# Optimization experiments

Measured on AMD Instinct MI355X. Metric: run time of the kernel, lower is better.

The kernel has to match this reference:

```python
import jax, jax.numpy as jnp
import numpy as np

SUBSTEP = 10
FRAMES = 24
T = FRAMES * SUBSTEP
DT = 1.0 / 60.0 / SUBSTEP
SLOPE_DEG = 20.0
COS_S = float(np.cos(np.deg2rad(SLOPE_DEG)))
SIN_S = float(np.sin(np.deg2rad(SLOPE_DEG)))
INIT_HEIGHT = 0.1
N_VERTS = 2_000_000
GRAVITY = jnp.array([0.0, -9.8, 0.0], dtype=jnp.float32)
CONTACT_N = jnp.array([-SIN_S, COS_S, 0.0], dtype=jnp.float32)
EPS = 1e-6


def quat_mul(a, b):
    w1, x1, y1, z1 = a[0], a[1], a[2], a[3]
    w2, x2, y2, z2 = b[0], b[1], b[2], b[3]
    return jnp.stack([
        w1 * w2 - x1 * x2 - y1 * y2 - z1 * z2,
        w1 * x2 + x1 * w2 + y1 * z2 - z1 * y2,
        w1 * y2 + y1 * w2 + z1 * x2 - x1 * z2,
        w1 * z2 + z1 * w2 + x1 * y2 - y1 * x2,
    ])


def quat_to_matrix(q):
    q = q / jnp.linalg.norm(q)
    w, x, y, z = q[0], q[1], q[2], q[3]
    return jnp.stack([
        jnp.stack([1 - 2 * y * y - 2 * z * z, 2 * x * y - 2 * w * z, 2 * x * z + 2 * w * y]),
        jnp.stack([2 * x * y + 2 * w * z, 1 - 2 * x * x - 2 * z * z, 2 * y * z - 2 * w * x]),
        jnp.stack([2 * x * z - 2 * w * y, 2 * y * z + 2 * w * x, 1 - 2 * x * x - 2 * y * y]),
    ])


def cross_matrix(a):
    z = jnp.zeros((), dtype=a.dtype)
    return jnp.stack([
        jnp.stack([z, -a[2], a[1]]),
        jnp.stack([a[2], z, -a[0]]),
        jnp.stack([-a[1], a[0], z]),
    ])


def setup_inputs() -> dict:
    key = jax.random.key(0)
    k1, k2, k3 = jax.random.split(key, 3)
    return {
        "x": jax.random.normal(k1, (N_VERTS, 3), dtype=jnp.float32) * 0.2,
        "mass_center": jnp.zeros((3,), dtype=jnp.float32),
        "init_trans": jax.random.normal(k2, (3,), dtype=jnp.float32) * 0.3 + jnp.array([0.3, 0.5, 0.0]),
        "init_quat": jnp.ones((4,), dtype=jnp.float32),
        "init_v": jax.random.normal(k3, (3,), dtype=jnp.float32) * 0.1,
        "kn": jnp.array([0.5], dtype=jnp.float32),
        "mu": jnp.array([0.4], dtype=jnp.float32),
        "linear_damping": jnp.array([0.999], dtype=jnp.float32),
        "angular_damping": jnp.array([0.998], dtype=jnp.float32),
    }


def _simulate(x, mass_center, init_trans, init_quat, init_v, kn, mu, linear_damping, angular_damping):
    n = x.shape[0]
    mass = jnp.asarray(float(n), dtype=x.dtype)  # unit mass per vertex
    inv_mass = 1.0 / mass
    r = x - mass_center
    # inertia_reference = sum_i m*( (r.r) I - outer(r,r) )
    inertia = jnp.sum(jnp.einsum('ni,ni->n', r, r)) * jnp.eye(3, dtype=x.dtype) - jnp.einsum('ni,nj->ij', r, r)
    kn0, mu0 = kn[0], mu[0]
    ld, ad = linear_damping[0], angular_damping[0]
    eye3 = jnp.eye(3, dtype=x.dtype)

    def step(carry, _):
        trans, quat, v, omega = carry
        Rm = quat_to_matrix(quat)
        Rx = x @ Rm.T                                   # [N,3]
        xi = trans + Rx + mass_center                   # world positions
        vi_all = v + jnp.cross(omega[None, :], Rx)      # per-vertex velocities
        d = xi @ CONTACT_N
        rel_v = vi_all @ CONTACT_N
        mask = (d < -COS_S * INIT_HEIGHT) & (rel_v < 0.0)
        num = jnp.sum(mask)
        numf = jnp.maximum(num, 1).astype(x.dtype)
        sum_pos = jnp.sum(x * mask[:, None].astype(x.dtype), axis=0)
        ri = sum_pos / numf
        Ri = Rm @ ri
        vi = v + jnp.cross(omega, Ri)
        v_n = jnp.dot(vi, CONTACT_N) * CONTACT_N
        v_t = vi - v_n
        vn_new = -kn0 * v_n
        alpha = jnp.maximum(1.0 - mu0 * (1.0 + kn0) * (jnp.linalg.norm(v_n) / (jnp.linalg.norm(v_t) + EPS)), 0.0)
        vi_new = vn_new + alpha * v_t
        I = Rm @ inertia @ Rm.T
        I_inv = jnp.linalg.inv(I)
        Rri = cross_matrix(Ri)
        kmat = inv_mass * eye3 - Rri @ I_inv @ Rri
        J = jnp.linalg.solve(kmat, vi_new - vi)
        hit = num > 0
        dv = jnp.where(hit, J * inv_mass, 0.0)
        domega = jnp.where(hit, I_inv @ Rri @ J, 0.0)
        v_new = (v + GRAVITY * DT) * ld + dv
        omega_new = omega * ad + domega
        trans_new = trans + DT * v_new
        wq = jnp.concatenate([jnp.zeros((1,), dtype=x.dtype), omega_new]) * (0.5 * DT)
        quat_new = quat + quat_mul(wq, quat)
        quat_new = quat_new / jnp.linalg.norm(quat_new)
        new_carry = (trans_new, quat_new, v_new, omega_new)
        return new_carry, jnp.concatenate([trans_new, quat_new])

    carry0 = (init_trans, init_quat / jnp.linalg.norm(init_quat), init_v, jnp.zeros(3, dtype=x.dtype))
    _, traj = jax.lax.scan(step, carry0, None, length=T)
    return traj  # [T, 7] = translation(3) + quaternion(4) per substep


def reference(x, mass_center, init_trans, init_quat, init_v, kn, mu, linear_damping, angular_damping):
    return _simulate(x, mass_center, init_trans, init_quat, init_v, kn, mu, linear_damping, angular_damping)
```

## Files before the change

kernel.cpp:

```cpp
#include <hip/hip_runtime.h>

#define GRID    256
#define BLOCK   512
#define NWAVES  (BLOCK / 64)
#define CHUNK   7813

typedef unsigned long long u64;

__device__ __forceinline__ u64 rec_load(const u64* p) {
  return __hip_atomic_load(p, __ATOMIC_RELAXED, __HIP_MEMORY_SCOPE_AGENT);
}
__device__ __forceinline__ void rec_store(u64* p, u64 v) {
  __hip_atomic_store(p, v, __ATOMIC_RELAXED, __HIP_MEMORY_SCOPE_AGENT);
}
__device__ __forceinline__ u64 rec_pack(float f, unsigned tag) {
  return (u64)__float_as_uint(f) | ((u64)tag << 32);
}

template <int NV>
__device__ __forceinline__ void block_reduce(float* v, float* sm) {
  #pragma unroll
  for (int off = 32; off > 0; off >>= 1) {
    #pragma unroll
    for (int k = 0; k < NV; ++k) v[k] += __shfl_down(v[k], off, 64);
  }
  const int lane = threadIdx.x & 63;
  const int wid  = threadIdx.x >> 6;
  if (lane == 0) {
    #pragma unroll
    for (int k = 0; k < NV; ++k) sm[wid * NV + k] = v[k];
  }
  __syncthreads();
  if (threadIdx.x == 0) {
    #pragma unroll
    for (int w = 1; w < NWAVES; ++w) {
      #pragma unroll
      for (int k = 0; k < NV; ++k) v[k] += sm[w * NV + k];
    }
  }
  __syncthreads();
}

__device__ __forceinline__ void mat3_mul(const float* A, const float* B, float* C) {
  #pragma unroll
  for (int i = 0; i < 3; ++i)
    #pragma unroll
    for (int j = 0; j < 3; ++j)
      C[i*3+j] = A[i*3+0]*B[0*3+j] + A[i*3+1]*B[1*3+j] + A[i*3+2]*B[2*3+j];
}
__device__ __forceinline__ void mat3_mul_bt(const float* A, const float* B, float* C) {
  #pragma unroll
  for (int i = 0; i < 3; ++i)
    #pragma unroll
    for (int j = 0; j < 3; ++j)
      C[i*3+j] = A[i*3+0]*B[j*3+0] + A[i*3+1]*B[j*3+1] + A[i*3+2]*B[j*3+2];
}
__device__ __forceinline__ void mat3_inv(const float* m, float* inv) {
  float A =  (m[4]*m[8] - m[5]*m[7]);
  float B = -(m[3]*m[8] - m[5]*m[6]);
  float C =  (m[3]*m[7] - m[4]*m[6]);
  float det = m[0]*A + m[1]*B + m[2]*C;
  float id = 1.0f / det;
  inv[0] = A * id;
  inv[1] = -(m[1]*m[8] - m[2]*m[7]) * id;
  inv[2] =  (m[1]*m[5] - m[2]*m[4]) * id;
  inv[3] = B * id;
  inv[4] =  (m[0]*m[8] - m[2]*m[6]) * id;
  inv[5] = -(m[0]*m[5] - m[2]*m[3]) * id;
  inv[6] = C * id;
  inv[7] = -(m[0]*m[7] - m[1]*m[6]) * id;
  inv[8] =  (m[0]*m[4] - m[1]*m[3]) * id;
}

__global__ __launch_bounds__(BLOCK)
void sim_kernel(const float* __restrict__ xg,
                const float* __restrict__ mc_p,
                const float* __restrict__ itr_p,
                const float* __restrict__ iq_p,
                const float* __restrict__ iv_p,
                const float* __restrict__ kn_p,
                const float* __restrict__ mu_p,
                const float* __restrict__ ldp_p,
                const float* __restrict__ adp_p,
                float* __restrict__ out,
                u64* __restrict__ ws,
                int N, int T)
{
  const int tid = threadIdx.x;
  const int bid = blockIdx.x;

  extern __shared__ float dyn[];
  float* sXx = dyn;
  float* sXy = dyn + CHUNK;
  float* sXz = dyn + 2 * CHUNK;
  __shared__ float s_red[NWAVES * 8];
  __shared__ float s_plane[8];

  const float nx  = (float)(-0.3420201433256687);
  const float ny  = (float)( 0.9396926207859084);
  const float DTF = (float)(1.0 / 60.0 / 10.0);
  const float HDT = (float)(0.5 * (1.0 / 60.0 / 10.0));
  const float DTH = (float)(-0.9396926207859084 * 0.1);
  const float GYDT = -9.8f * (float)(1.0 / 60.0 / 10.0);

  const float mc0 = mc_p[0], mc1 = mc_p[1], mc2 = mc_p[2];

  u64* part0 = ws;
  u64* part1 = ws + 4 * GRID;
  u64* st    = ws + 8 * GRID;
  u64* bufI  = ws + 8 * GRID + 128;

  const int vstart = bid * CHUNK;
  int cl = N - vstart; if (cl > CHUNK) cl = CHUNK; if (cl < 0) cl = 0;

  for (int i = tid; i < cl; i += BLOCK) {
    const float* p = xg + (size_t)(vstart + i) * 3;
    sXx[i] = p[0]; sXy[i] = p[1]; sXz[i] = p[2];
  }
  __syncthreads();

  {
    float v6[6] = {0,0,0,0,0,0};
    for (int i = tid; i < cl; i += BLOCK) {
      float r0 = sXx[i] - mc0, r1 = sXy[i] - mc1, r2 = sXz[i] - mc2;
      v6[0] += r0*r0; v6[1] += r1*r1; v6[2] += r2*r2;
      v6[3] += r0*r1; v6[4] += r0*r2; v6[5] += r1*r2;
    }
    block_reduce<6>(v6, s_red);
    if (tid == 0) {
      #pragma unroll
      for (int k = 0; k < 6; ++k) rec_store(bufI + k * GRID + bid, rec_pack(v6[k], 0xC0FFEEu));
    }
  }

  float In[9];
  if (bid == 0) {
    float v6[6] = {0,0,0,0,0,0};
    if (tid < GRID) {
      u64 r[6];
      int f = 0;
      for (;;) {
        #pragma unroll
        for (int k = 0; k < 6; ++k) r[k] = rec_load(bufI + k * GRID + tid);
        bool ok = true;
        #pragma unroll
        for (int k = 0; k < 6; ++k) ok &= ((unsigned)(r[k] >> 32) == 0xC0FFEEu);
        if (ok) break;
        if ((++f & 15) == 0) __builtin_amdgcn_s_sleep(1);
      }
      #pragma unroll
      for (int k = 0; k < 6; ++k) v6[k] = __uint_as_float((unsigned)r[k]);
    }
    block_reduce<6>(v6, s_red);
    float trc = v6[0] + v6[1] + v6[2];
    In[0] = trc - v6[0]; In[4] = trc - v6[1]; In[8] = trc - v6[2];
    In[1] = -v6[3]; In[3] = -v6[3];
    In[2] = -v6[4]; In[6] = -v6[4];
    In[5] = -v6[5]; In[7] = -v6[5];
  }

  float tr0 = itr_p[0], tr1 = itr_p[1], tr2 = itr_p[2];
  float q0 = iq_p[0], q1 = iq_p[1], q2 = iq_p[2], q3 = iq_p[3];
  {
    float n0 = sqrtf(q0*q0 + q1*q1 + q2*q2 + q3*q3);
    q0 /= n0; q1 /= n0; q2 /= n0; q3 /= n0;
  }
  float v0 = iv_p[0], v1 = iv_p[1], v2 = iv_p[2];
  float om0 = 0.f, om1 = 0.f, om2 = 0.f;
  const float knv = kn_p[0], muv = mu_p[0], ldv = ldp_p[0], adv = adp_p[0];
  const float inv_mass = 1.0f / (float)N;

  float Rm[9];
  float Ii[9];

  if (tid == 0) {
    float qn = sqrtf(q0*q0 + q1*q1 + q2*q2 + q3*q3);
    float w = q0/qn, xq = q1/qn, yq = q2/qn, zq = q3/qn;
    Rm[0] = 1.f - 2.f*yq*yq - 2.f*zq*zq; Rm[1] = 2.f*xq*yq - 2.f*w*zq; Rm[2] = 2.f*xq*zq + 2.f*w*yq;
    Rm[3] = 2.f*xq*yq + 2.f*w*zq; Rm[4] = 1.f - 2.f*xq*xq - 2.f*zq*zq; Rm[5] = 2.f*yq*zq - 2.f*w*xq;
    Rm[6] = 2.f*xq*zq - 2.f*w*yq; Rm[7] = 2.f*yq*zq + 2.f*w*xq; Rm[8] = 1.f - 2.f*xq*xq - 2.f*yq*yq;
    float a0 = Rm[0]*nx + Rm[3]*ny;
    float a1 = Rm[1]*nx + Rm[4]*ny;
    float a2 = Rm[2]*nx + Rm[5]*ny;
    float w0 = ny*om2, w1 = -nx*om2, w2 = nx*om1 - ny*om0;
    float b0 = Rm[0]*w0 + Rm[3]*w1 + Rm[6]*w2;
    float b1 = Rm[1]*w0 + Rm[4]*w1 + Rm[7]*w2;
    float b2 = Rm[2]*w0 + Rm[5]*w1 + Rm[8]*w2;
    float ca = DTH - ((tr0 + mc0)*nx + (tr1 + mc1)*ny);
    float cb = -(v0*nx + v1*ny);
    s_plane[0] = a0; s_plane[1] = a1; s_plane[2] = a2;
    s_plane[3] = b0; s_plane[4] = b1; s_plane[5] = b2;
    s_plane[6] = ca; s_plane[7] = cb;
    if (bid == 0) {
      float Tm[9]; mat3_mul(Rm, In, Tm);
      float Iw[9]; mat3_mul_bt(Tm, Rm, Iw);
      mat3_inv(Iw, Ii);
    }
  }
  __syncthreads();

  for (int t = 0; t < T; ++t) {
    const float a0 = s_plane[0], a1 = s_plane[1], a2 = s_plane[2];
    const float b0 = s_plane[3], b1 = s_plane[4], b2 = s_plane[5];
    const float ca = s_plane[6], cb = s_plane[7];

    float acc[4] = {0.f, 0.f, 0.f, 0.f};
    for (int i = tid; i < cl; i += BLOCK) {
      float x0 = sXx[i], x1 = sXy[i], x2 = sXz[i];
      float da = x0*a0 + x1*a1 + x2*a2;
      float db = x0*b0 + x1*b1 + x2*b2;
      if (da < ca && db < cb) { acc[0] += 1.f; acc[1] += x0; acc[2] += x1; acc[3] += x2; }
    }
    block_reduce<4>(acc, s_red);

    const unsigned want = (unsigned)(t + 1);
    u64* pb = (t & 1) ? part1 : part0;
    if (tid == 0) {
      #pragma unroll
      for (int k = 0; k < 4; ++k) rec_store(pb + k * GRID + bid, rec_pack(acc[k], want));
    }

    if (bid == 0) {
      float tot[4] = {0.f, 0.f, 0.f, 0.f};
      if (tid < GRID) {
        u64 r0, r1, r2, r3;
        int f = 0;
        for (;;) {
          r0 = rec_load(pb + 0 * GRID + tid);
          r1 = rec_load(pb + 1 * GRID + tid);
          r2 = rec_load(pb + 2 * GRID + tid);
          r3 = rec_load(pb + 3 * GRID + tid);
          if ((unsigned)(r0 >> 32) == want && (unsigned)(r1 >> 32) == want &&
              (unsigned)(r2 >> 32) == want && (unsigned)(r3 >> 32) == want) break;
          if ((++f & 15) == 0) __builtin_amdgcn_s_sleep(1);
        }
        tot[0] = __uint_as_float((unsigned)r0);
        tot[1] = __uint_as_float((unsigned)r1);
        tot[2] = __uint_as_float((unsigned)r2);
        tot[3] = __uint_as_float((unsigned)r3);
      }
      block_reduce<4>(tot, s_red);

      if (tid == 0) {
        float num = tot[0];
        float numf = fmaxf(num, 1.0f);
        float ri0 = tot[1] / numf, ri1 = tot[2] / numf, ri2 = tot[3] / numf;
        float Ri0 = Rm[0]*ri0 + Rm[1]*ri1 + Rm[2]*ri2;
        float Ri1 = Rm[3]*ri0 + Rm[4]*ri1 + Rm[5]*ri2;
        float Ri2 = Rm[6]*ri0 + Rm[7]*ri1 + Rm[8]*ri2;
        float dv0 = 0.f, dv1 = 0.f, dv2 = 0.f, dm0 = 0.f, dm1 = 0.f, dm2 = 0.f;
        if (num > 0.0f) {
          float vi0 = v0 + om1*Ri2 - om2*Ri1;
          float vi1 = v1 + om2*Ri0 - om0*Ri2;
          float vi2 = v2 + om0*Ri1 - om1*Ri0;
          float vdn = vi0*nx + vi1*ny;
          float vn0 = vdn*nx, vn1 = vdn*ny;
          float vt0 = vi0 - vn0, vt1 = vi1 - vn1, vt2 = vi2;
          float nvn = sqrtf(vn0*vn0 + vn1*vn1);
          float nvt = sqrtf(vt0*vt0 + vt1*vt1 + vt2*vt2);
          float alpha = fmaxf(1.0f - muv*(1.0f + knv)*(nvn/(nvt + 1e-6f)), 0.0f);
          float dvi0 = (-knv*vn0 + alpha*vt0) - vi0;
          float dvi1 = (-knv*vn1 + alpha*vt1) - vi1;
          float dvi2 = (alpha*vt2) - vi2;
          float Cx[9] = {0.f, -Ri2, Ri1,  Ri2, 0.f, -Ri0,  -Ri1, Ri0, 0.f};
          float T2[9]; mat3_mul(Cx, Ii, T2);
          float T3[9]; mat3_mul(T2, Cx, T3);
          float K[9];
          #pragma unroll
          for (int k = 0; k < 9; ++k) K[k] = -T3[k];
          K[0] += inv_mass; K[4] += inv_mass; K[8] += inv_mass;
          float Ki[9]; mat3_inv(K, Ki);
          float J0 = Ki[0]*dvi0 + Ki[1]*dvi1 + Ki[2]*dvi2;
          float J1 = Ki[3]*dvi0 + Ki[4]*dvi1 + Ki[5]*dvi2;
          float J2 = Ki[6]*dvi0 + Ki[7]*dvi1 + Ki[8]*dvi2;
          dv0 = J0*inv_mass; dv1 = J1*inv_mass; dv2 = J2*inv_mass;
          float c0 = -Ri2*J1 + Ri1*J2;
          float c1 =  Ri2*J0 - Ri0*J2;
          float c2 = -Ri1*J0 + Ri0*J1;
          dm0 = Ii[0]*c0 + Ii[1]*c1 + Ii[2]*c2;
          dm1 = Ii[3]*c0 + Ii[4]*c1 + Ii[5]*c2;
          dm2 = Ii[6]*c0 + Ii[7]*c1 + Ii[8]*c2;
        }
        v0 = v0*ldv + dv0;
        v1 = (v1 + GYDT)*ldv + dv1;
        v2 = v2*ldv + dv2;
        om0 = om0*adv + dm0; om1 = om1*adv + dm1; om2 = om2*adv + dm2;
        tr0 = tr0 + DTF*v0; tr1 = tr1 + DTF*v1; tr2 = tr2 + DTF*v2;
        float wx = om0*HDT, wy = om1*HDT, wz = om2*HDT;
        float dq0 = -wx*q1 - wy*q2 - wz*q3;
        float dq1 =  wx*q0 + wy*q3 - wz*q2;
        float dq2 =  wy*q0 + wz*q1 - wx*q3;
        float dq3 =  wz*q0 + wx*q2 - wy*q1;
        q0 += dq0; q1 += dq1; q2 += dq2; q3 += dq3;
        float qn2 = sqrtf(q0*q0 + q1*q1 + q2*q2 + q3*q3);
        q0 /= qn2; q1 /= qn2; q2 /= qn2; q3 /= qn2;
        float* o = out + (size_t)t * 7;
        o[0] = tr0; o[1] = tr1; o[2] = tr2;
        o[3] = q0;  o[4] = q1;  o[5] = q2;  o[6] = q3;
        float qn = sqrtf(q0*q0 + q1*q1 + q2*q2 + q3*q3);
        float w = q0/qn, xq = q1/qn, yq = q2/qn, zq = q3/qn;
        Rm[0] = 1.f - 2.f*yq*yq - 2.f*zq*zq; Rm[1] = 2.f*xq*yq - 2.f*w*zq; Rm[2] = 2.f*xq*zq + 2.f*w*yq;
        Rm[3] = 2.f*xq*yq + 2.f*w*zq; Rm[4] = 1.f - 2.f*xq*xq - 2.f*zq*zq; Rm[5] = 2.f*yq*zq - 2.f*w*xq;
        Rm[6] = 2.f*xq*zq - 2.f*w*yq; Rm[7] = 2.f*yq*zq + 2.f*w*xq; Rm[8] = 1.f - 2.f*xq*xq - 2.f*yq*yq;
        float na0 = Rm[0]*nx + Rm[3]*ny;
        float na1 = Rm[1]*nx + Rm[4]*ny;
        float na2 = Rm[2]*nx + Rm[5]*ny;
        float w0 = ny*om2, w1 = -nx*om2, w2 = nx*om1 - ny*om0;
        float nb0 = Rm[0]*w0 + Rm[3]*w1 + Rm[6]*w2;
        float nb1 = Rm[1]*w0 + Rm[4]*w1 + Rm[7]*w2;
        float nb2 = Rm[2]*w0 + Rm[5]*w1 + Rm[8]*w2;
        float nca = DTH - ((tr0 + mc0)*nx + (tr1 + mc1)*ny);
        float ncb = -(v0*nx + v1*ny);
        s_plane[0] = na0; s_plane[1] = na1; s_plane[2] = na2;
        s_plane[3] = nb0; s_plane[4] = nb1; s_plane[5] = nb2;
        s_plane[6] = nca; s_plane[7] = ncb;
      }
      __syncthreads();
      if (tid < 64) {
        u64* sl = st + (size_t)((t + 1) & 1) * 64;
        rec_store(sl + tid, rec_pack(s_plane[tid & 7], want));
      }
      if (tid == 0) {
        float Tm[9]; mat3_mul(Rm, In, Tm);
        float Iw[9]; mat3_mul_bt(Tm, Rm, Iw);
        mat3_inv(Iw, Ii);
      }
    } else {
      if (tid < 8) {
        const u64* sl = st + (size_t)((t + 1) & 1) * 64 + (size_t)(bid & 7) * 8;
        u64 r; int f = 0;
        for (;;) {
          r = rec_load(sl + tid);
          if ((unsigned)(r >> 32) == want) break;
          if ((++f & 31) == 0) __builtin_amdgcn_s_sleep(1);
        }
        s_plane[tid] = __uint_as_float((unsigned)r);
      }
      __syncthreads();
    }
  }
}

extern "C" void kernel_launch(void* const* d_in, const int* in_sizes, int n_in,
                              void* d_out, int out_size, void* d_ws, size_t ws_size,
                              hipStream_t stream) {
  const float* x   = (const float*)d_in[0];
  const float* mc  = (const float*)d_in[1];
  const float* itr = (const float*)d_in[2];
  const float* iq  = (const float*)d_in[3];
  const float* iv  = (const float*)d_in[4];
  const float* kn  = (const float*)d_in[5];
  const float* mu  = (const float*)d_in[6];
  const float* ldp = (const float*)d_in[7];
  const float* adp = (const float*)d_in[8];
  float* out = (float*)d_out;
  u64* ws  = (u64*)d_ws;
  int N = in_sizes[0] / 3;
  int T = out_size / 7;

  const int dyn_lds = 3 * CHUNK * 4;
  hipFuncSetAttribute((const void*)sim_kernel,
                      hipFuncAttributeMaxDynamicSharedMemorySize, dyn_lds);

  void* args[] = {(void*)&x, (void*)&mc, (void*)&itr, (void*)&iq, (void*)&iv,
                  (void*)&kn, (void*)&mu, (void*)&ldp, (void*)&adp,
                  (void*)&out, (void*)&ws, (void*)&N, (void*)&T};
  hipLaunchCooperativeKernel((void*)sim_kernel, dim3(GRID), dim3(BLOCK),
                             args, dyn_lds, stream);
}
```

Measured before the change: 1.469 ms.

## Dedicate block 0 to a single-wave coordinator, distribute vertices over remaining blocks

Block 0 no longer processes vertices. Its first wave polls all partial records, reduces them with wave shuffles, integrates the rigid body and publishes the next plane, with no __syncthreads or LDS round trips on the serial critical path. The other 255 blocks take slightly larger chunks to cover all vertices. This shortens the per-step serial latency between the global reduction and the broadcast, at the cost of one idle block and a little more work per compute block.

```diff
diff --git a/kernel.cpp b/kernel.cpp
--- a/kernel.cpp
+++ b/kernel.cpp
@@ -3,7 +3,7 @@
 #define GRID    256
 #define BLOCK   512
 #define NWAVES  (BLOCK / 64)
-#define CHUNK   7813
+#define CHUNK   7844
 
 typedef unsigned long long u64;
 
@@ -86,8 +86,10 @@
                 u64* __restrict__ ws,
                 int N, int T)
 {
-  const int tid = threadIdx.x;
-  const int bid = blockIdx.x;
+  const int tid  = threadIdx.x;
+  const int bid  = blockIdx.x;
+  const int lane = tid & 63;
+  const int wid  = tid >> 6;
 
   extern __shared__ float dyn[];
   float* sXx = dyn;
@@ -110,8 +112,9 @@
   u64* st    = ws + 8 * GRID;
   u64* bufI  = ws + 8 * GRID + 128;
 
-  const int vstart = bid * CHUNK;
-  int cl = N - vstart; if (cl > CHUNK) cl = CHUNK; if (cl < 0) cl = 0;
+  const int vstart = (bid - 1) * CHUNK;
+  int cl = 0;
+  if (bid > 0) { cl = N - vstart; if (cl > CHUNK) cl = CHUNK; if (cl < 0) cl = 0; }
 
   for (int i = tid; i < cl; i += BLOCK) {
     const float* p = xg + (size_t)(vstart + i) * 3;
@@ -199,133 +202,167 @@
   }
   __syncthreads();
 
-  for (int t = 0; t < T; ++t) {
-    const float a0 = s_plane[0], a1 = s_plane[1], a2 = s_plane[2];
-    const float b0 = s_plane[3], b1 = s_plane[4], b2 = s_plane[5];
-    const float ca = s_plane[6], cb = s_plane[7];
-
-    float acc[4] = {0.f, 0.f, 0.f, 0.f};
-    for (int i = tid; i < cl; i += BLOCK) {
-      float x0 = sXx[i], x1 = sXy[i], x2 = sXz[i];
-      float da = x0*a0 + x1*a1 + x2*a2;
-      float db = x0*b0 + x1*b1 + x2*b2;
-      if (da < ca && db < cb) { acc[0] += 1.f; acc[1] += x0; acc[2] += x1; acc[3] += x2; }
-    }
-    block_reduce<4>(acc, s_red);
-
-    const unsigned want = (unsigned)(t + 1);
-    u64* pb = (t & 1) ? part1 : part0;
-    if (tid == 0) {
-      #pragma unroll
-      for (int k = 0; k < 4; ++k) rec_store(pb + k * GRID + bid, rec_pack(acc[k], want));
-    }
-
-    if (bid == 0) {
-      float tot[4] = {0.f, 0.f, 0.f, 0.f};
-      if (tid < GRID) {
-        u64 r0, r1, r2, r3;
-        int f = 0;
-        for (;;) {
-          r0 = rec_load(pb + 0 * GRID + tid);
-          r1 = rec_load(pb + 1 * GRID + tid);
-          r2 = rec_load(pb + 2 * GRID + tid);
-          r3 = rec_load(pb + 3 * GRID + tid);
-          if ((unsigned)(r0 >> 32) == want && (unsigned)(r1 >> 32) == want &&
-              (unsigned)(r2 >> 32) == want && (unsigned)(r3 >> 32) == want) break;
-          if ((++f & 15) == 0) __builtin_amdgcn_s_sleep(1);
-        }
-        tot[0] = __uint_as_float((unsigned)r0);
-        tot[1] = __uint_as_float((unsigned)r1);
-        tot[2] = __uint_as_float((unsigned)r2);
-        tot[3] = __uint_as_float((unsigned)r3);
+  if (bid == 0) {
+    if (wid == 0) {
+      const int base = lane * 4;
+      for (int t = 0; t < T; ++t) {
+        const unsigned want = (unsigned)(t + 1);
+        u64* pb = (t & 1) ? part1 : part0;
+
+        u64 r0_[4], r1_[4], r2_[4], r3_[4];
+        {
+          int f = 0;
+          for (;;) {
+            #pragma unroll
+            for (int j = 0; j < 4; ++j) {
+              r0_[j] = rec_load(pb + 0 * GRID + base + j);
+              r1_[j] = rec_load(pb + 1 * GRID + base + j);
+              r2_[j] = rec_load(pb + 2 * GRID + base + j);
+              r3_[j] = rec_load(pb + 3 * GRID + base + j);
+            }
+            bool ok = true;
+            #pragma unroll
+            for (int j = 0; j < 4; ++j) {
+              bool skip = (base + j == 0);
+              ok &= skip || (((unsigned)(r0_[j] >> 32) == want) &&
+                             ((unsigned)(r1_[j] >> 32) == want) &&
+                             ((unsigned)(r2_[j] >> 32) == want) &&
+                             ((unsigned)(r3_[j] >> 32) == want));
+            }
+            if (__ballot(ok) == ~0ull) break;
+            if ((++f & 15) == 0) __builtin_amdgcn_s_sleep(1);
+          }
+        }
+        float s0 = 0.f, s1 = 0.f, s2 = 0.f, s3 = 0.f;
+        #pragma unroll
+        for (int j = 0; j < 4; ++j) {
+          if (base + j != 0) {
+            s0 += __uint_as_float((unsigned)r0_[j]);
+            s1 += __uint_as_float((unsigned)r1_[j]);
+            s2 += __uint_as_float((unsigned)r2_[j]);
+            s3 += __uint_as_float((unsigned)r3_[j]);
+          }
+        }
+        #pragma unroll
+        for (int off = 32; off > 0; off >>= 1) {
+          s0 += __shfl_down(s0, off, 64);
+          s1 += __shfl_down(s1, off, 64);
+          s2 += __shfl_down(s2, off, 64);
+          s3 += __shfl_down(s3, off, 64);
+        }
+
+        float pl0, pl1, pl2, pl3, pl4, pl5, pl6, pl7;
+        if (lane == 0) {
+          float num = s0;
+          float numf = fmaxf(num, 1.0f);
+          float ri0 = s1 / numf, ri1 = s2 / numf, ri2 = s3 / numf;
+          float Ri0 = Rm[0]*ri0 + Rm[1]*ri1 + Rm[2]*ri2;
+          float Ri1 = Rm[3]*ri0 + Rm[4]*ri1 + Rm[5]*ri2;
+          float Ri2 = Rm[6]*ri0 + Rm[7]*ri1 + Rm[8]*ri2;
+          float dv0 = 0.f, dv1 = 0.f, dv2 = 0.f, dm0 = 0.f, dm1 = 0.f, dm2 = 0.f;
+          if (num > 0.0f) {
+            float vi0 = v0 + om1*Ri2 - om2*Ri1;
+            float vi1 = v1 + om2*Ri0 - om0*Ri2;
+            float vi2 = v2 + om0*Ri1 - om1*Ri0;
+            float vdn = vi0*nx + vi1*ny;
+            float vn0 = vdn*nx, vn1 = vdn*ny;
+            float vt0 = vi0 - vn0, vt1 = vi1 - vn1, vt2 = vi2;
+            float nvn = sqrtf(vn0*vn0 + vn1*vn1);
+            float nvt = sqrtf(vt0*vt0 + vt1*vt1 + vt2*vt2);
+            float alpha = fmaxf(1.0f - muv*(1.0f + knv)*(nvn/(nvt + 1e-6f)), 0.0f);
+            float dvi0 = (-knv*vn0 + alpha*vt0) - vi0;
+            float dvi1 = (-knv*vn1 + alpha*vt1) - vi1;
+            float dvi2 = (alpha*vt2) - vi2;
+            float Cx[9] = {0.f, -Ri2, Ri1,  Ri2, 0.f, -Ri0,  -Ri1, Ri0, 0.f};
+            float T2[9]; mat3_mul(Cx, Ii, T2);
+            float T3[9]; mat3_mul(T2, Cx, T3);
+            float K[9];
+            #pragma unroll
+            for (int k = 0; k < 9; ++k) K[k] = -T3[k];
+            K[0] += inv_mass; K[4] += inv_mass; K[8] += inv_mass;
+            float Ki[9]; mat3_inv(K, Ki);
+            float J0 = Ki[0]*dvi0 + Ki[1]*dvi1 + Ki[2]*dvi2;
+            float J1 = Ki[3]*dvi0 + Ki[4]*dvi1 + Ki[5]*dvi2;
+            float J2 = Ki[6]*dvi0 + Ki[7]*dvi1 + Ki[8]*dvi2;
+            dv0 = J0*inv_mass; dv1 = J1*inv_mass; dv2 = J2*inv_mass;
+            float c0 = -Ri2*J1 + Ri1*J2;
+            float c1 =  Ri2*J0 - Ri0*J2;
+            float c2 = -Ri1*J0 + Ri0*J1;
+            dm0 = Ii[0]*c0 + Ii[1]*c1 + Ii[2]*c2;
+            dm1 = Ii[3]*c0 + Ii[4]*c1 + Ii[5]*c2;
+            dm2 = Ii[6]*c0 + Ii[7]*c1 + Ii[8]*c2;
+          }
+          v0 = v0*ldv + dv0;
+          v1 = (v1 + GYDT)*ldv + dv1;
+          v2 = v2*ldv + dv2;
+          om0 = om0*adv + dm0; om1 = om1*adv + dm1; om2 = om2*adv + dm2;
+          tr0 = tr0 + DTF*v0; tr1 = tr1 + DTF*v1; tr2 = tr2 + DTF*v2;
+          float wx = om0*HDT, wy = om1*HDT, wz = om2*HDT;
+          float dq0 = -wx*q1 - wy*q2 - wz*q3;
+          float dq1 =  wx*q0 + wy*q3 - wz*q2;
+          float dq2 =  wy*q0 + wz*q1 - wx*q3;
+          float dq3 =  wz*q0 + wx*q2 - wy*q1;
+          q0 += dq0; q1 += dq1; q2 += dq2; q3 += dq3;
+          float qn2 = sqrtf(q0*q0 + q1*q1 + q2*q2 + q3*q3);
+          q0 /= qn2; q1 /= qn2; q2 /= qn2; q3 /= qn2;
+          float qn = sqrtf(q0*q0 + q1*q1 + q2*q2 + q3*q3);
+          float w = q0/qn, xq = q1/qn, yq = q2/qn, zq = q3/qn;
+          Rm[0] = 1.f - 2.f*yq*yq - 2.f*zq*zq; Rm[1] = 2.f*xq*yq - 2.f*w*zq; Rm[2] = 2.f*xq*zq + 2.f*w*yq;
+          Rm[3] = 2.f*xq*yq + 2.f*w*zq; Rm[4] = 1.f - 2.f*xq*xq - 2.f*zq*zq; Rm[5] = 2.f*yq*zq - 2.f*w*xq;
+          Rm[6] = 2.f*xq*zq - 2.f*w*yq; Rm[7] = 2.f*yq*zq + 2.f*w*xq; Rm[8] = 1.f - 2.f*xq*xq - 2.f*yq*yq;
+          pl0 = Rm[0]*nx + Rm[3]*ny;
+          pl1 = Rm[1]*nx + Rm[4]*ny;
+          pl2 = Rm[2]*nx + Rm[5]*ny;
+          float w0 = ny*om2, w1 = -nx*om2, w2 = nx*om1 - ny*om0;
+          pl3 = Rm[0]*w0 + Rm[3]*w1 + Rm[6]*w2;
+          pl4 = Rm[1]*w0 + Rm[4]*w1 + Rm[7]*w2;
+          pl5 = Rm[2]*w0 + Rm[5]*w1 + Rm[8]*w2;
+          pl6 = DTH - ((tr0 + mc0)*nx + (tr1 + mc1)*ny);
+          pl7 = -(v0*nx + v1*ny);
+        }
+
+        float b0v = __shfl(pl0, 0, 64), b1v = __shfl(pl1, 0, 64);
+        float b2v = __shfl(pl2, 0, 64), b3v = __shfl(pl3, 0, 64);
+        float b4v = __shfl(pl4, 0, 64), b5v = __shfl(pl5, 0, 64);
+        float b6v = __shfl(pl6, 0, 64), b7v = __shfl(pl7, 0, 64);
+        int k = lane & 7;
+        float mine = (k == 0) ? b0v : (k == 1) ? b1v : (k == 2) ? b2v : (k == 3) ? b3v
+                   : (k == 4) ? b4v : (k == 5) ? b5v : (k == 6) ? b6v : b7v;
+        u64* sl = st + (size_t)((t + 1) & 1) * 64;
+        rec_store(sl + lane, rec_pack(mine, want));
+
+        if (lane == 0) {
+          float* o = out + (size_t)t * 7;
+          o[0] = tr0; o[1] = tr1; o[2] = tr2;
+          o[3] = q0;  o[4] = q1;  o[5] = q2;  o[6] = q3;
+          float Tm[9]; mat3_mul(Rm, In, Tm);
+          float Iw[9]; mat3_mul_bt(Tm, Rm, Iw);
+          mat3_inv(Iw, Ii);
+        }
       }
-      block_reduce<4>(tot, s_red);
-
+    }
+  } else {
+    for (int t = 0; t < T; ++t) {
+      const float a0 = s_plane[0], a1 = s_plane[1], a2 = s_plane[2];
+      const float b0 = s_plane[3], b1 = s_plane[4], b2 = s_plane[5];
+      const float ca = s_plane[6], cb = s_plane[7];
+
+      float acc[4] = {0.f, 0.f, 0.f, 0.f};
+      for (int i = tid; i < cl; i += BLOCK) {
+        float x0 = sXx[i], x1 = sXy[i], x2 = sXz[i];
+        float da = x0*a0 + x1*a1 + x2*a2;
+        float db = x0*b0 + x1*b1 + x2*b2;
+        if (da < ca && db < cb) { acc[0] += 1.f; acc[1] += x0; acc[2] += x1; acc[3] += x2; }
+      }
+      block_reduce<4>(acc, s_red);
+
+      const unsigned want = (unsigned)(t + 1);
+      u64* pb = (t & 1) ? part1 : part0;
       if (tid == 0) {
-        float num = tot[0];
-        float numf = fmaxf(num, 1.0f);
-        float ri0 = tot[1] / numf, ri1 = tot[2] / numf, ri2 = tot[3] / numf;
-        float Ri0 = Rm[0]*ri0 + Rm[1]*ri1 + Rm[2]*ri2;
-        float Ri1 = Rm[3]*ri0 + Rm[4]*ri1 + Rm[5]*ri2;
-        float Ri2 = Rm[6]*ri0 + Rm[7]*ri1 + Rm[8]*ri2;
-        float dv0 = 0.f, dv1 = 0.f, dv2 = 0.f, dm0 = 0.f, dm1 = 0.f, dm2 = 0.f;
-        if (num > 0.0f) {
-          float vi0 = v0 + om1*Ri2 - om2*Ri1;
-          float vi1 = v1 + om2*Ri0 - om0*Ri2;
-          float vi2 = v2 + om0*Ri1 - om1*Ri0;
-          float vdn = vi0*nx + vi1*ny;
-          float vn0 = vdn*nx, vn1 = vdn*ny;
-          float vt0 = vi0 - vn0, vt1 = vi1 - vn1, vt2 = vi2;
-          float nvn = sqrtf(vn0*vn0 + vn1*vn1);
-          float nvt = sqrtf(vt0*vt0 + vt1*vt1 + vt2*vt2);
-          float alpha = fmaxf(1.0f - muv*(1.0f + knv)*(nvn/(nvt + 1e-6f)), 0.0f);
-          float dvi0 = (-knv*vn0 + alpha*vt0) - vi0;
-          float dvi1 = (-knv*vn1 + alpha*vt1) - vi1;
-          float dvi2 = (alpha*vt2) - vi2;
-          float Cx[9] = {0.f, -Ri2, Ri1,  Ri2, 0.f, -Ri0,  -Ri1, Ri0, 0.f};
-          float T2[9]; mat3_mul(Cx, Ii, T2);
-          float T3[9]; mat3_mul(T2, Cx, T3);
-          float K[9];
-          #pragma unroll
-          for (int k = 0; k < 9; ++k) K[k] = -T3[k];
-          K[0] += inv_mass; K[4] += inv_mass; K[8] += inv_mass;
-          float Ki[9]; mat3_inv(K, Ki);
-          float J0 = Ki[0]*dvi0 + Ki[1]*dvi1 + Ki[2]*dvi2;
-          float J1 = Ki[3]*dvi0 + Ki[4]*dvi1 + Ki[5]*dvi2;
-          float J2 = Ki[6]*dvi0 + Ki[7]*dvi1 + Ki[8]*dvi2;
-          dv0 = J0*inv_mass; dv1 = J1*inv_mass; dv2 = J2*inv_mass;
-          float c0 = -Ri2*J1 + Ri1*J2;
-          float c1 =  Ri2*J0 - Ri0*J2;
-          float c2 = -Ri1*J0 + Ri0*J1;
-          dm0 = Ii[0]*c0 + Ii[1]*c1 + Ii[2]*c2;
-          dm1 = Ii[3]*c0 + Ii[4]*c1 + Ii[5]*c2;
-          dm2 = Ii[6]*c0 + Ii[7]*c1 + Ii[8]*c2;
-        }
-        v0 = v0*ldv + dv0;
-        v1 = (v1 + GYDT)*ldv + dv1;
-        v2 = v2*ldv + dv2;
-        om0 = om0*adv + dm0; om1 = om1*adv + dm1; om2 = om2*adv + dm2;
-        tr0 = tr0 + DTF*v0; tr1 = tr1 + DTF*v1; tr2 = tr2 + DTF*v2;
-        float wx = om0*HDT, wy = om1*HDT, wz = om2*HDT;
-        float dq0 = -wx*q1 - wy*q2 - wz*q3;
-        float dq1 =  wx*q0 + wy*q3 - wz*q2;
-        float dq2 =  wy*q0 + wz*q1 - wx*q3;
-        float dq3 =  wz*q0 + wx*q2 - wy*q1;
-        q0 += dq0; q1 += dq1; q2 += dq2; q3 += dq3;
-        float qn2 = sqrtf(q0*q0 + q1*q1 + q2*q2 + q3*q3);
-        q0 /= qn2; q1 /= qn2; q2 /= qn2; q3 /= qn2;
-        float* o = out + (size_t)t * 7;
-        o[0] = tr0; o[1] = tr1; o[2] = tr2;
-        o[3] = q0;  o[4] = q1;  o[5] = q2;  o[6] = q3;
-        float qn = sqrtf(q0*q0 + q1*q1 + q2*q2 + q3*q3);
-        float w = q0/qn, xq = q1/qn, yq = q2/qn, zq = q3/qn;
-        Rm[0] = 1.f - 2.f*yq*yq - 2.f*zq*zq; Rm[1] = 2.f*xq*yq - 2.f*w*zq; Rm[2] = 2.f*xq*zq + 2.f*w*yq;
-        Rm[3] = 2.f*xq*yq + 2.f*w*zq; Rm[4] = 1.f - 2.f*xq*xq - 2.f*zq*zq; Rm[5] = 2.f*yq*zq - 2.f*w*xq;
-        Rm[6] = 2.f*xq*zq - 2.f*w*yq; Rm[7] = 2.f*yq*zq + 2.f*w*xq; Rm[8] = 1.f - 2.f*xq*xq - 2.f*yq*yq;
-        float na0 = Rm[0]*nx + Rm[3]*ny;
-        float na1 = Rm[1]*nx + Rm[4]*ny;
-        float na2 = Rm[2]*nx + Rm[5]*ny;
-        float w0 = ny*om2, w1 = -nx*om2, w2 = nx*om1 - ny*om0;
-        float nb0 = Rm[0]*w0 + Rm[3]*w1 + Rm[6]*w2;
-        float nb1 = Rm[1]*w0 + Rm[4]*w1 + Rm[7]*w2;
-        float nb2 = Rm[2]*w0 + Rm[5]*w1 + Rm[8]*w2;
-        float nca = DTH - ((tr0 + mc0)*nx + (tr1 + mc1)*ny);
-        float ncb = -(v0*nx + v1*ny);
-        s_plane[0] = na0; s_plane[1] = na1; s_plane[2] = na2;
-        s_plane[3] = nb0; s_plane[4] = nb1; s_plane[5] = nb2;
-        s_plane[6] = nca; s_plane[7] = ncb;
+        #pragma unroll
+        for (int k = 0; k < 4; ++k) rec_store(pb + k * GRID + bid, rec_pack(acc[k], want));
       }
-      __syncthreads();
-      if (tid < 64) {
-        u64* sl = st + (size_t)((t + 1) & 1) * 64;
-        rec_store(sl + tid, rec_pack(s_plane[tid & 7], want));
-      }
-      if (tid == 0) {
-        float Tm[9]; mat3_mul(Rm, In, Tm);
-        float Iw[9]; mat3_mul_bt(Tm, Rm, Iw);
-        mat3_inv(Iw, Ii);
-      }
-    } else {
+
       if (tid < 8) {
         const u64* sl = st + (size_t)((t + 1) & 1) * 64 + (size_t)(bid & 7) * 8;
         u64 r; int f = 0;
```

Result: slower. 1.579 ms (+7.5%).
